# Kernel optimization log

Measured on AMD Instinct MI355X. Metric: run time of the kernel, lower is better.

Reference implementation:

```python
import jax, jax.numpy as jnp
import numpy as np

EMBED = 1024
ATTN = 1024

def setup_inputs() -> dict:
    key = jax.random.key(0)
    k1, k2, k3, k4 = jax.random.split(key, 4)
    x = jax.random.normal(k1, (32, 2048, EMBED), dtype=jnp.float32)
    W = jax.random.normal(k2, (EMBED, ATTN), dtype=jnp.float32) / np.sqrt(EMBED)
    b = jax.random.normal(k3, (ATTN,), dtype=jnp.float32) * 0.01
    ctx = jax.random.normal(k4, (ATTN,), dtype=jnp.float32)
    return {"x": x, "W": W, "b": b, "ctx": ctx}

def reference(x, W, b, ctx):
    # scores: [B, S] = tanh(x @ W + b) . ctx
    h = jnp.tanh(jnp.einsum('bse,ea->bsa', x, W) + b)
    scores = jnp.einsum('bsa,a->bs', h, ctx)
    weights = jax.nn.softmax(scores, axis=1)            # softmax over seq dim
    return jnp.einsum('bse,bs->be', x, weights)          # weighted sum pooling
```

## Files before the change

kernel.cpp:

```cpp
#include <hip/hip_runtime.h>
#include <hip/hip_bf16.h>

typedef _Float16 half8 __attribute__((ext_vector_type(8)));
typedef _Float16 half4 __attribute__((ext_vector_type(4)));
typedef float floatx4 __attribute__((ext_vector_type(4)));

#define EMBED 1024
#define SEQ   2048
#define BATCH 32
#define M_TOT (BATCH * SEQ)
#define KDIM  1024
#define NDIM  1024

#define GLOAD16(g, l) __builtin_amdgcn_global_load_lds(                      \
    (const __attribute__((address_space(1))) void*)(g),                      \
    (__attribute__((address_space(3))) void*)(l), 16, 0, 0)

__global__ void transpose_w_kernel(const float* __restrict__ W,
                                   _Float16* __restrict__ Wt) {
    __shared__ float t[32][33];
    const int kt = blockIdx.x * 32;
    const int nt = blockIdx.y * 32;
    #pragma unroll
    for (int i = 0; i < 4; ++i)
        t[threadIdx.y + 8 * i][threadIdx.x] =
            W[(size_t)(kt + threadIdx.y + 8 * i) * NDIM + nt + threadIdx.x];
    __syncthreads();
    #pragma unroll
    for (int i = 0; i < 4; ++i)
        Wt[(size_t)(nt + threadIdx.y + 8 * i) * KDIM + kt + threadIdx.x] =
            (_Float16)t[threadIdx.x][threadIdx.y + 8 * i];
}

__global__ void zero_kernel(float* __restrict__ scores, float* __restrict__ out) {
    const int i = blockIdx.x * 256 + threadIdx.x;
    if (i < M_TOT) scores[i] = 0.0f;
    if (i < BATCH * EMBED) out[i] = 0.0f;
}

__global__ __launch_bounds__(256) void cvt_x_kernel(const float* __restrict__ x,
                                                    _Float16* __restrict__ x16) {
    const size_t stride = (size_t)gridDim.x * 256 * 8;
    for (size_t i = ((size_t)blockIdx.x * 256 + threadIdx.x) * 8;
         i < (size_t)M_TOT * KDIM; i += stride) {
        const float4 a = *(const float4*)(x + i);
        const float4 b = *(const float4*)(x + i + 4);
        half8 h;
        h[0] = (_Float16)a.x; h[1] = (_Float16)a.y; h[2] = (_Float16)a.z; h[3] = (_Float16)a.w;
        h[4] = (_Float16)b.x; h[5] = (_Float16)b.y; h[6] = (_Float16)b.z; h[7] = (_Float16)b.w;
        *(half8*)(x16 + i) = h;
    }
}

__global__ __launch_bounds__(512, 2) void score_gemm4(
    const _Float16* __restrict__ x16, const _Float16* __restrict__ Wt,
    const float* __restrict__ bias, const float* __restrict__ ctx,
    float* __restrict__ scores) {
    __shared__ _Float16 As[2][256 * 64];
    __shared__ _Float16 Bs[2][256 * 64];

    const int tid = threadIdx.x;
    const int lane = tid & 63;
    const int w = tid >> 6;
    const int wm = w >> 2;
    const int wn = w & 3;

    const int nb = ((blockIdx.x & 7) << 7) | (blockIdx.x >> 3);
    const int bm = nb >> 2;
    const int bn = nb & 3;

    const int srow  = lane >> 3;
    const int sslot = (lane & 7) ^ srow;
    const _Float16* Ab = x16 + (size_t)(bm * 256) * KDIM;
    const _Float16* Bb = Wt  + (size_t)(bn * 256) * KDIM;

    #define STAGE(buf, kt)                                                         \
        {                                                                          \
            _Pragma("unroll")                                                      \
            for (int i = 0; i < 4; ++i) {                                          \
                const int j = i * 8 + w;                                           \
                const size_t go = (size_t)(j * 8 + srow) * KDIM + (kt) * 64 + sslot * 8; \
                GLOAD16(Ab + go, &As[buf][j * 512]);                               \
                GLOAD16(Bb + go, &Bs[buf][j * 512]);                               \
            }                                                                      \
        }

    const int frow = lane & 15;
    const int fsw  = frow & 7;
    const int fhi  = lane >> 4;

    floatx4 acc[8][4] = {};

    STAGE(0, 0);
    __syncthreads();

    for (int kt = 0; kt < 16; ++kt) {
        const int cur = kt & 1;
        if (kt < 15) STAGE(cur ^ 1, kt + 1);

        #pragma unroll
        for (int ks = 0; ks < 2; ++ks) {
            const int sp = ks * 4 + fhi;
            half8 bfr[4];
            #pragma unroll
            for (int ni = 0; ni < 4; ++ni) {
                const int r = wn * 64 + ni * 16 + frow;
                bfr[ni] = *(const half8*)&Bs[cur][r * 64 + ((sp ^ fsw) * 8)];
            }
            __builtin_amdgcn_s_setprio(1);
            #pragma unroll
            for (int mi = 0; mi < 8; ++mi) {
                const int r = wm * 128 + mi * 16 + frow;
                const half8 a = *(const half8*)&As[cur][r * 64 + ((sp ^ fsw) * 8)];
                #pragma unroll
                for (int ni = 0; ni < 4; ++ni)
                    acc[mi][ni] = __builtin_amdgcn_mfma_f32_16x16x32_f16(
                        a, bfr[ni], acc[mi][ni], 0, 0, 0);
            }
            __builtin_amdgcn_s_setprio(0);
        }
        __syncthreads();
    }
    #undef STAGE

    float bv[4], cv[4];
    #pragma unroll
    for (int ni = 0; ni < 4; ++ni) {
        const int col = bn * 256 + wn * 64 + ni * 16 + frow;
        bv[ni] = bias[col];
        cv[ni] = ctx[col];
    }
    #pragma unroll
    for (int mi = 0; mi < 8; ++mi) {
        #pragma unroll
        for (int j = 0; j < 4; ++j) {
            float partial = 0.0f;
            #pragma unroll
            for (int ni = 0; ni < 4; ++ni) {
                const float v = acc[mi][ni][j] + bv[ni];
                const float e = __expf(2.0f * v);
                const float t = 1.0f - 2.0f * __builtin_amdgcn_rcpf(e + 1.0f);
                partial += t * cv[ni];
            }
            #pragma unroll
            for (int off = 1; off < 16; off <<= 1)
                partial += __shfl_xor(partial, off, 64);
            if (frow == 0) {
                const int rowg = bm * 256 + wm * 128 + mi * 16 + fhi * 4 + j;
                atomicAdd(&scores[rowg], partial);
            }
        }
    }
}

__global__ __launch_bounds__(256) void score_gemm_f32(
    const float* __restrict__ A32p, const _Float16* __restrict__ Wt,
    const float* __restrict__ bias, const float* __restrict__ ctx,
    float* __restrict__ scores) {
    __shared__ _Float16 As[128 * 64];
    __shared__ _Float16 Bs[128 * 64];

    const int bid = blockIdx.x;
    const int bm = bid >> 3;
    const int bn = bid & 7;
    const int tid = threadIdx.x;
    const int lane = tid & 63;
    const int wid = tid >> 6;
    const int wm = wid >> 1;
    const int wn = wid & 1;

    const int c = tid & 7;
    const int r0 = tid >> 3;
    const int swz = (r0 & 7) << 3;
    const int wcol = (c * 8) ^ swz;

    float4 aF[4][2];
    int4   bR[4];

    #pragma unroll
    for (int i = 0; i < 4; ++i) {
        const int row = r0 + 32 * i;
        const float* p = A32p + (size_t)(bm * 128 + row) * KDIM + c * 8;
        aF[i][0] = *(const float4*)p;
        aF[i][1] = *(const float4*)(p + 4);
        bR[i] = *(const int4*)(Wt + (size_t)(bn * 128 + row) * KDIM + c * 8);
    }

    floatx4 acc[4][4] = {};

    for (int kt = 0; kt < KDIM / 64; ++kt) {
        __syncthreads();
        #pragma unroll
        for (int i = 0; i < 4; ++i) {
            const int row = r0 + 32 * i;
            half8 h;
            h[0] = (_Float16)aF[i][0].x; h[1] = (_Float16)aF[i][0].y;
            h[2] = (_Float16)aF[i][0].z; h[3] = (_Float16)aF[i][0].w;
            h[4] = (_Float16)aF[i][1].x; h[5] = (_Float16)aF[i][1].y;
            h[6] = (_Float16)aF[i][1].z; h[7] = (_Float16)aF[i][1].w;
            *(half8*)&As[row * 64 + wcol] = h;
            *(int4*)&Bs[row * 64 + wcol] = bR[i];
        }
        __syncthreads();

        if (kt + 1 < KDIM / 64) {
            #pragma unroll
            for (int i = 0; i < 4; ++i) {
                const int row = r0 + 32 * i;
                const float* p = A32p + (size_t)(bm * 128 + row) * KDIM + (kt + 1) * 64 + c * 8;
                aF[i][0] = *(const float4*)p;
                aF[i][1] = *(const float4*)(p + 4);
                bR[i] = *(const int4*)(Wt + (size_t)(bn * 128 + row) * KDIM + (kt + 1) * 64 + c * 8);
            }
        }

        #pragma unroll
        for (int s = 0; s < 2; ++s) {
            half8 afr[4], bfr[4];
            const int colr = s * 32 + (lane >> 4) * 8;
            #pragma unroll
            for (int m = 0; m < 4; ++m) {
                const int row = wm * 64 + m * 16 + (lane & 15);
                afr[m] = *(const half8*)&As[row * 64 + (colr ^ ((row & 7) << 3))];
            }
            #pragma unroll
            for (int n = 0; n < 4; ++n) {
                const int row = wn * 64 + n * 16 + (lane & 15);
                bfr[n] = *(const half8*)&Bs[row * 64 + (colr ^ ((row & 7) << 3))];
            }
            #pragma unroll
            for (int m = 0; m < 4; ++m)
                #pragma unroll
                for (int n = 0; n < 4; ++n)
                    acc[m][n] = __builtin_amdgcn_mfma_f32_16x16x32_f16(
                        afr[m], bfr[n], acc[m][n], 0, 0, 0);
        }
    }

    float bv[4], cv[4];
    #pragma unroll
    for (int n = 0; n < 4; ++n) {
        const int col = bn * 128 + wn * 64 + n * 16 + (lane & 15);
        bv[n] = bias[col];
        cv[n] = ctx[col];
    }
    #pragma unroll
    for (int m = 0; m < 4; ++m) {
        #pragma unroll
        for (int j = 0; j < 4; ++j) {
            float partial = 0.0f;
            #pragma unroll
            for (int n = 0; n < 4; ++n) {
                const float v = acc[m][n][j] + bv[n];
                const float e = __expf(2.0f * v);
                const float t = 1.0f - 2.0f * __builtin_amdgcn_rcpf(e + 1.0f);
                partial += t * cv[n];
            }
            #pragma unroll
            for (int off = 1; off < 16; off <<= 1)
                partial += __shfl_xor(partial, off, 64);
            if ((lane & 15) == 0) {
                const int rowg = bm * 128 + wm * 64 + m * 16 + (lane >> 4) * 4 + j;
                atomicAdd(&scores[rowg], partial);
            }
        }
    }
}

__global__ void softmax_kernel(const float* __restrict__ scores,
                               float* __restrict__ weights) {
    const int bb = blockIdx.x;
    const int tid = threadIdx.x;
    const float* s = scores + (size_t)bb * SEQ;
    float* w = weights + (size_t)bb * SEQ;

    __shared__ float red[8];

    float v[8];
    float mx = -1e30f;
    #pragma unroll
    for (int i = 0; i < 8; ++i) {
        v[i] = s[tid + i * 256];
        mx = fmaxf(mx, v[i]);
    }
    #pragma unroll
    for (int off = 1; off < 64; off <<= 1)
        mx = fmaxf(mx, __shfl_xor(mx, off, 64));
    const int wv = tid >> 6;
    if ((tid & 63) == 0) red[wv] = mx;
    __syncthreads();
    mx = fmaxf(fmaxf(red[0], red[1]), fmaxf(red[2], red[3]));

    float sum = 0.0f;
    #pragma unroll
    for (int i = 0; i < 8; ++i) {
        v[i] = __expf(v[i] - mx);
        sum += v[i];
    }
    #pragma unroll
    for (int off = 1; off < 64; off <<= 1)
        sum += __shfl_xor(sum, off, 64);
    if ((tid & 63) == 0) red[4 + wv] = sum;
    __syncthreads();
    sum = red[4] + red[5] + red[6] + red[7];
    const float inv = 1.0f / sum;
    #pragma unroll
    for (int i = 0; i < 8; ++i)
        w[tid + i * 256] = v[i] * inv;
}

__global__ __launch_bounds__(256) void pool_kernel(const float* __restrict__ x,
                                                   const float* __restrict__ weights,
                                                   float* __restrict__ out) {
    const int bb = blockIdx.x >> 4;
    const int sc = blockIdx.x & 15;
    const int tid = threadIdx.x;

    const float4* xb = (const float4*)(x + (size_t)bb * SEQ * EMBED) +
                       (size_t)(sc * 128) * (EMBED / 4) + tid;
    const float* wb = weights + (size_t)bb * SEQ + sc * 128;

    float ax = 0.f, ay = 0.f, az = 0.f, aw = 0.f;
    #pragma unroll 4
    for (int s = 0; s < 128; ++s) {
        const float wgt = wb[s];
        const float4 xv = xb[(size_t)s * (EMBED / 4)];
        ax += wgt * xv.x; ay += wgt * xv.y; az += wgt * xv.z; aw += wgt * xv.w;
    }
    float* o = out + (size_t)bb * EMBED + tid * 4;
    atomicAdd(o + 0, ax);
    atomicAdd(o + 1, ay);
    atomicAdd(o + 2, az);
    atomicAdd(o + 3, aw);
}

__global__ __launch_bounds__(256) void pool16_kernel(const _Float16* __restrict__ x16,
                                                     const float* __restrict__ weights,
                                                     float* __restrict__ out) {
    const int bb = blockIdx.x >> 4;
    const int sc = blockIdx.x & 15;
    const int tid = threadIdx.x;

    const _Float16* xb = x16 + (size_t)bb * SEQ * EMBED +
                         (size_t)(sc * 128) * EMBED + tid * 4;
    const float* wb = weights + (size_t)bb * SEQ + sc * 128;

    float ax = 0.f, ay = 0.f, az = 0.f, aw = 0.f;
    #pragma unroll 4
    for (int s = 0; s < 128; ++s) {
        const float wgt = wb[s];
        const half4 h = *(const half4*)(xb + (size_t)s * EMBED);
        ax += wgt * (float)h[0]; ay += wgt * (float)h[1];
        az += wgt * (float)h[2]; aw += wgt * (float)h[3];
    }
    float* o = out + (size_t)bb * EMBED + tid * 4;
    atomicAdd(o + 0, ax);
    atomicAdd(o + 1, ay);
    atomicAdd(o + 2, az);
    atomicAdd(o + 3, aw);
}

extern "C" void kernel_launch(void* const* d_in, const int* in_sizes, int n_in,
                              void* d_out, int out_size, void* d_ws, size_t ws_size,
                              hipStream_t stream) {
    const float* x   = (const float*)d_in[0];
    const float* W   = (const float*)d_in[1];
    const float* b   = (const float*)d_in[2];
    const float* ctx = (const float*)d_in[3];
    float* out = (float*)d_out;

    char* ws = (char*)d_ws;
    _Float16* Wt      = (_Float16*)ws;
    float*    scores  = (float*)(ws + (2u << 20));
    float*    weights = (float*)(ws + (2u << 20) + (256u << 10));
    _Float16* x16     = (_Float16*)(ws + (4u << 20));

    const size_t need = (4ull << 20) + ((size_t)M_TOT * KDIM * 2);
    const bool fast = ws_size >= need;

    hipLaunchKernelGGL(transpose_w_kernel, dim3(32, 32), dim3(32, 8), 0, stream, W, Wt);
    hipLaunchKernelGGL(zero_kernel, dim3(M_TOT / 256), dim3(256), 0, stream, scores, out);

    if (fast) {
        hipLaunchKernelGGL(cvt_x_kernel, dim3(4096), dim3(256), 0, stream, x, x16);
        hipLaunchKernelGGL(score_gemm4, dim3(1024), dim3(512), 0, stream,
                           x16, Wt, b, ctx, scores);
    } else {
        hipLaunchKernelGGL(score_gemm_f32, dim3(4096), dim3(256), 0, stream,
                           x, Wt, b, ctx, scores);
    }

    hipLaunchKernelGGL(softmax_kernel, dim3(BATCH), dim3(256), 0, stream, scores, weights);

    if (fast) {
        hipLaunchKernelGGL(pool16_kernel, dim3(BATCH * 16), dim3(256), 0, stream,
                           x16, weights, out);
    } else {
        hipLaunchKernelGGL(pool_kernel, dim3(BATCH * 16), dim3(256), 0, stream,
                           x, weights, out);
    }
}
```

Baseline: 293.1 us.

## Interleave fine-grained LDS staging with MFMA phases in score GEMM

Rewrites the score GEMM main loop as a manually scheduled, 8-phase ping-pong pipeline. Each k-tile is split into four MFMA sub-phases separated by raw s_barrier, with the async global-to-LDS loads for the next tile spread between them and gated by explicit vmcnt waits. The LDS layout is split by warp-row halves so each warp stages only the rows it needs. This is meant to hide global load latency and LDS traffic behind MFMA work, at the cost of many more barriers and fragile hand-written waitcnt ordering.

```diff
diff --git a/kernel.cpp b/kernel.cpp
--- a/kernel.cpp
+++ b/kernel.cpp
@@ -52,76 +52,114 @@
     }
 }
 
-__global__ __launch_bounds__(512, 2) void score_gemm4(
+__global__ __launch_bounds__(512, 2) void score_gemm5(
     const _Float16* __restrict__ x16, const _Float16* __restrict__ Wt,
     const float* __restrict__ bias, const float* __restrict__ ctx,
     float* __restrict__ scores) {
-    __shared__ _Float16 As[2][256 * 64];
-    __shared__ _Float16 Bs[2][256 * 64];
-
-    const int tid = threadIdx.x;
+    __shared__ _Float16 As[2][2][128 * 64];
+    __shared__ _Float16 Bs[2][2][128 * 64];
+
+    const int tid  = threadIdx.x;
     const int lane = tid & 63;
-    const int w = tid >> 6;
-    const int wm = w >> 2;
-    const int wn = w & 3;
+    const int w    = tid >> 6;
+    const int wm   = w >> 2;
+    const int wn   = w & 3;
+    const int wnh  = wn >> 1;
+    const int wnl  = wn & 1;
 
     const int nb = ((blockIdx.x & 7) << 7) | (blockIdx.x >> 3);
     const int bm = nb >> 2;
     const int bn = nb & 3;
 
     const int srow  = lane >> 3;
-    const int sslot = (lane & 7) ^ srow;
-    const _Float16* Ab = x16 + (size_t)(bm * 256) * KDIM;
-    const _Float16* Bb = Wt  + (size_t)(bn * 256) * KDIM;
-
-    #define STAGE(buf, kt)                                                         \
-        {                                                                          \
-            _Pragma("unroll")                                                      \
-            for (int i = 0; i < 4; ++i) {                                          \
-                const int j = i * 8 + w;                                           \
-                const size_t go = (size_t)(j * 8 + srow) * KDIM + (kt) * 64 + sslot * 8; \
-                GLOAD16(Ab + go, &As[buf][j * 512]);                               \
-                GLOAD16(Bb + go, &Bs[buf][j * 512]);                               \
-            }                                                                      \
-        }
+    const int gslot = (lane & 7) ^ srow;
+    const int q2    = wm * 2 + wnl;
+    const _Float16* Abase = x16 + (size_t)(bm * 256 + wm * 128 + wn * 32 + srow) * KDIM + gslot * 8;
+    const _Float16* Bbase = Wt  + (size_t)(bn * 256 + wnh * 128 + q2 * 32 + srow) * KDIM + gslot * 8;
+
+#define STAGE_A(d, kt1, i) GLOAD16(Abase + (size_t)(i) * 8 * KDIM + (kt1) * 64,  \
+                                   &As[d][wm][(wn * 32 + (i) * 8) * 64])
+#define STAGE_B(d, kt1, i) GLOAD16(Bbase + (size_t)(i) * 8 * KDIM + (kt1) * 64,  \
+                                   &Bs[d][wnh][(q2 * 32 + (i) * 8) * 64])
 
     const int frow = lane & 15;
-    const int fsw  = frow & 7;
     const int fhi  = lane >> 4;
+    const int fx   = frow & 7;
+
+#define LD_A4(c, ks, mi0)                                                       \
+    _Pragma("unroll")                                                           \
+    for (int m = 0; m < 4; ++m)                                                 \
+        afr[m] = *(const half8*)&As[c][wm][((mi0 + m) * 16 + frow) * 64 +       \
+                                           ((((ks) * 4 + fhi) ^ fx) * 8)];
+#define LD_B4(c, ks)                                                            \
+    _Pragma("unroll")                                                           \
+    for (int n = 0; n < 4; ++n)                                                 \
+        bfr[n] = *(const half8*)&Bs[c][wnh][(wnl * 64 + n * 16 + frow) * 64 +   \
+                                            ((((ks) * 4 + fhi) ^ fx) * 8)];
+#define MFMA16(mi0)                                                             \
+    __builtin_amdgcn_s_setprio(1);                                              \
+    _Pragma("unroll")                                                           \
+    for (int m = 0; m < 4; ++m)                                                 \
+        _Pragma("unroll")                                                       \
+        for (int n = 0; n < 4; ++n)                                             \
+            acc[mi0 + m][n] = __builtin_amdgcn_mfma_f32_16x16x32_f16(           \
+                afr[m], bfr[n], acc[mi0 + m][n], 0, 0, 0);                      \
+    __builtin_amdgcn_s_setprio(0);
+
+#define BAR() asm volatile("s_barrier" ::: "memory")
+
+#define KTILE(c, d, kt1, STG, VMW)                                              \
+    {                                                                           \
+                                                          \
+        if (STG) { STAGE_A(d, kt1, 0); STAGE_A(d, kt1, 1); }                    \
+        asm volatile(VMW ::: "memory");                                         \
+        BAR();                                                                  \
+        LD_B4(c, 0); LD_A4(c, 0, 0);                                            \
+        MFMA16(0);                                                              \
+        BAR();                                                                  \
+                                                          \
+        LD_A4(c, 0, 4);                                                         \
+        if (STG) { STAGE_A(d, kt1, 2); STAGE_A(d, kt1, 3); }                    \
+        BAR();                                                                  \
+        MFMA16(4);                                                              \
+        BAR();                                                                  \
+                                                            \
+        LD_B4(c, 1); LD_A4(c, 1, 0);                                            \
+        if (STG) { STAGE_B(d, kt1, 0); STAGE_B(d, kt1, 1); }                    \
+        BAR();                                                                  \
+        MFMA16(0 + 0);                                                          \
+        BAR();                                                                  \
+                                                            \
+        LD_A4(c, 1, 4);                                                         \
+        if (STG) { STAGE_B(d, kt1, 2); STAGE_B(d, kt1, 3); }                    \
+        BAR();                                                                  \
+        MFMA16(4);                                                              \
+        BAR();                                                                  \
+    }
 
     floatx4 acc[8][4] = {};
-
-    STAGE(0, 0);
-    __syncthreads();
-
-    for (int kt = 0; kt < 16; ++kt) {
-        const int cur = kt & 1;
-        if (kt < 15) STAGE(cur ^ 1, kt + 1);
-
-        #pragma unroll
-        for (int ks = 0; ks < 2; ++ks) {
-            const int sp = ks * 4 + fhi;
-            half8 bfr[4];
-            #pragma unroll
-            for (int ni = 0; ni < 4; ++ni) {
-                const int r = wn * 64 + ni * 16 + frow;
-                bfr[ni] = *(const half8*)&Bs[cur][r * 64 + ((sp ^ fsw) * 8)];
-            }
-            __builtin_amdgcn_s_setprio(1);
-            #pragma unroll
-            for (int mi = 0; mi < 8; ++mi) {
-                const int r = wm * 128 + mi * 16 + frow;
-                const half8 a = *(const half8*)&As[cur][r * 64 + ((sp ^ fsw) * 8)];
-                #pragma unroll
-                for (int ni = 0; ni < 4; ++ni)
-                    acc[mi][ni] = __builtin_amdgcn_mfma_f32_16x16x32_f16(
-                        a, bfr[ni], acc[mi][ni], 0, 0, 0);
-            }
-            __builtin_amdgcn_s_setprio(0);
-        }
-        __syncthreads();
-    }
-    #undef STAGE
+    half8 afr[4], bfr[4];
+
+    #pragma unroll
+    for (int i = 0; i < 4; ++i) STAGE_A(0, 0, i);
+    #pragma unroll
+    for (int i = 0; i < 4; ++i) STAGE_B(0, 0, i);
+
+    for (int kt2 = 0; kt2 < 7; ++kt2) {
+        const int kt = kt2 * 2;
+        KTILE(0, 1, kt + 1, 1, "s_waitcnt vmcnt(2)");
+        KTILE(1, 0, kt + 2, 1, "s_waitcnt vmcnt(2)");
+    }
+    KTILE(0, 1, 15, 1, "s_waitcnt vmcnt(2)");
+    KTILE(1, 0, 0, 0, "s_waitcnt vmcnt(0)");
+
+#undef KTILE
+#undef BAR
+#undef MFMA16
+#undef LD_B4
+#undef LD_A4
+#undef STAGE_B
+#undef STAGE_A
 
     float bv[4], cv[4];
     #pragma unroll
@@ -383,7 +421,7 @@
 
     if (fast) {
         hipLaunchKernelGGL(cvt_x_kernel, dim3(4096), dim3(256), 0, stream, x, x16);
-        hipLaunchKernelGGL(score_gemm4, dim3(1024), dim3(512), 0, stream,
+        hipLaunchKernelGGL(score_gemm5, dim3(1024), dim3(512), 0, stream,
                            x16, Wt, b, ctx, scores);
     } else {
         hipLaunchKernelGGL(score_gemm_f32, dim3(4096), dim3(256), 0, stream,
```

Result: no change. 287.9 us (-1.8%).
